# Kernel tuning notes

Measured on AMD Instinct MI355X. Metric: run time of the kernel, lower is better.

The kernel has to match this reference:

```python
import jax, jax.numpy as jnp
import numpy as np

B, T, M, DK, DV, S = 64, 256, 64, 128, 256, 128
NSK, NQ = 200, 2000


def _glorot(k, shape):
    lim = np.sqrt(6.0 / (shape[0] + shape[1])).astype(np.float32)
    return jax.random.uniform(k, shape, jnp.float32, -lim, lim)


def setup_inputs() -> dict:
    key = jax.random.key(0)
    ks = jax.random.split(key, 16)
    tn = lambda k, shape: 0.1 * jax.random.truncated_normal(k, -2.0, 2.0, shape, jnp.float32)
    return {
        "q_data": jax.random.randint(ks[0], (B, T), 0, NSK + 1),
        "qa_data": jax.random.randint(ks[1], (B, T), 0, 2 * NSK + 1),
        "s_data": jax.random.randint(ks[2], (B, T), 0, NQ + 1),
        "key_memory": tn(ks[3], (M, DK)),
        "value_memory": tn(ks[4], (M, DV)),
        "Eq": 0.05 * jax.random.normal(ks[5], (NSK + 1, DK), jnp.float32),
        "Eqa": 0.05 * jax.random.normal(ks[6], (2 * NSK + 1, DV), jnp.float32),
        "Es": 0.05 * jax.random.normal(ks[7], (NQ + 1, DK), jnp.float32),
        "We": _glorot(ks[8], (DV, DV)), "be": jnp.zeros((DV,), jnp.float32),
        "Wa": _glorot(ks[9], (DV, DV)), "ba": jnp.zeros((DV,), jnp.float32),
        "Wsa": _glorot(ks[10], (DV, M)), "bsa": jnp.zeros((M,), jnp.float32),
        "Wqd1": _glorot(ks[11], (DK, S)), "bqd1": jnp.zeros((S,), jnp.float32),
        "Wqd": _glorot(ks[12], (S, 1)), "bqd": jnp.zeros((1,), jnp.float32),
        "Wsd1": _glorot(ks[13], (DK, S)), "bsd1": jnp.zeros((S,), jnp.float32),
        "Wsd": _glorot(ks[14], (S, 1)), "bsd": jnp.zeros((1,), jnp.float32),
    }


def reference(q_data, qa_data, s_data, key_memory, value_memory, Eq, Eqa, Es,
              We, be, Wa, ba, Wsa, bsa, Wqd1, bqd1, Wqd, bqd, Wsd1, bsd1, Wsd, bsd):
    b = q_data.shape[0]
    qe = Eq[q_data]    # [B,T,DK]
    qae = Eqa[qa_data]  # [B,T,DV]
    se = Es[s_data]    # [B,T,DK]
    # time-independent precomputation (same math, hoisted out of the loop)
    corr = jax.nn.softmax(jnp.einsum("btk,mk->btm", qe, key_memory), axis=-1)  # [B,T,M]
    erase = qae @ We + be  # [B,T,DV] (activation=None in source)
    add = qae @ Wa + ba    # [B,T,DV]
    qd = jnp.tanh(qe @ Wqd1 + bqd1) @ Wqd + bqd  # [B,T,1]
    sd = jnp.tanh(se @ Wsd1 + bsd1) @ Wsd + bsd  # [B,T,1]

    def step(Mv, x):
        cw, er, ad = x  # [B,M], [B,DV], [B,DV]
        read = jnp.einsum("bm,bmd->bd", cw, Mv)        # read BEFORE write
        sa1 = read @ Wsa + bsa                          # [B,M]
        sa = jnp.sum(cw * sa1, axis=1)                  # [B]
        scale = cw[:, :, None]                          # [B,M,1]
        Mv_new = Mv * (1.0 - er[:, None, :] * scale) + ad[:, None, :] * scale
        return Mv_new, sa

    Mv0 = jnp.broadcast_to(value_memory[None], (b,) + value_memory.shape)
    xs = (corr.transpose(1, 0, 2), erase.transpose(1, 0, 2), add.transpose(1, 0, 2))
    _, sa_t = jax.lax.scan(step, Mv0, xs)  # sa_t: [T,B]
    z = 3.0 * sa_t.T - qd[..., 0] - sd[..., 0]  # [B,T]
    return jax.nn.sigmoid(z)
```

## Files before the change

kernel.cpp:

```cpp
#include <hip/hip_runtime.h>
#include <math.h>

#define B_   64
#define T_   256
#define M_   64
#define DK_  128
#define DV_  256
#define S_   128
#define NQR  201
#define NQAR 401
#define NSR  2001

static __device__ __forceinline__ int imin(int a, int b){ return a < b ? a : b; }

static __device__ __forceinline__ float fast_tanh(float x){
  float e = __expf(2.f * x);
  return 1.f - 2.f / (e + 1.f);
}

template<int CTRL, int RM>
static __device__ __forceinline__ float dppadd(float x) {
  return x + __int_as_float(
      __builtin_amdgcn_update_dpp(0, __float_as_int(x), CTRL, RM, 0xf, true));
}
static __device__ __forceinline__ float wave_sum_lane63(float x) {
  x = dppadd<0x111, 0xf>(x);
  x = dppadd<0x112, 0xf>(x);
  x = dppadd<0x114, 0xf>(x);
  x = dppadd<0x118, 0xf>(x);
  x = dppadd<0x142, 0xa>(x);
  x = dppadd<0x143, 0xc>(x);
  return x;
}
static __device__ __forceinline__ float row_sum_lane15(float x) {
  x = dppadd<0x111, 0xf>(x);
  x = dppadd<0x112, 0xf>(x);
  x = dppadd<0x114, 0xf>(x);
  x = dppadd<0x118, 0xf>(x);
  return x;
}

__device__ void corr_role(int blk, const float* __restrict__ Eq,
                          const float* __restrict__ Km,
                          const float* __restrict__ Wsa,
                          const float* __restrict__ bsa,
                          float* __restrict__ corr,
                          float* __restrict__ w2_t,
                          float* __restrict__ csb_t)
{
  __shared__ float eq[4][DK_];
  __shared__ float cwb[4][M_];
  const int w = threadIdx.x >> 6, m = threadIdx.x & 63;
  const int i  = blk * 4 + w;
  const int ic = imin(i, NQR - 1);
  eq[w][m]      = Eq[ic * DK_ + m];
  eq[w][m + 64] = Eq[ic * DK_ + 64 + m];
  float acc = 0.f;
  const float4* kr = (const float4*)(Km + m * DK_);
  #pragma unroll 8
  for (int k4 = 0; k4 < DK_ / 4; ++k4) {
    float4 kv = kr[k4];
    acc = fmaf(eq[w][k4 * 4 + 0], kv.x, acc);
    acc = fmaf(eq[w][k4 * 4 + 1], kv.y, acc);
    acc = fmaf(eq[w][k4 * 4 + 2], kv.z, acc);
    acc = fmaf(eq[w][k4 * 4 + 3], kv.w, acc);
  }
  float mx = acc;
  #pragma unroll
  for (int off = 32; off; off >>= 1) mx = fmaxf(mx, __shfl_xor(mx, off, 64));
  float e = __expf(acc - mx);
  float ssum = e;
  #pragma unroll
  for (int off = 32; off; off >>= 1) ssum += __shfl_xor(ssum, off, 64);
  const float cw = e / ssum;
  if (i < NQR) corr[i * M_ + m] = cw;
  cwb[w][m] = cw;

  float pv = wave_sum_lane63(cw * bsa[m]);
  if (m == 63 && i < NQR) csb_t[i] = pv;

  float aw[4] = {0,0,0,0};
  for (int mm4 = 0; mm4 < M_ / 4; ++mm4) {
    #pragma unroll
    for (int r = 0; r < 4; ++r) {
      float4 wv = *(const float4*)(Wsa + (r * 64 + m) * M_ + mm4 * 4);
      aw[r] = fmaf(cwb[w][mm4 * 4 + 0], wv.x, aw[r]);
      aw[r] = fmaf(cwb[w][mm4 * 4 + 1], wv.y, aw[r]);
      aw[r] = fmaf(cwb[w][mm4 * 4 + 2], wv.z, aw[r]);
      aw[r] = fmaf(cwb[w][mm4 * 4 + 3], wv.w, aw[r]);
    }
  }
  if (i < NQR) {
    #pragma unroll
    for (int r = 0; r < 4; ++r) w2_t[i * DV_ + r * 64 + m] = aw[r];
  }
}

__device__ void ea_role(int blk, const float* __restrict__ Eqa,
                        const float* __restrict__ We, const float* __restrict__ be,
                        const float* __restrict__ Wa, const float* __restrict__ ba,
                        float* __restrict__ ert, float* __restrict__ adt)
{
  __shared__ float a[8][DV_];
  const int d  = threadIdx.x;
  const int i0 = blk * 8;
  #pragma unroll
  for (int r = 0; r < 8; ++r) a[r][d] = Eqa[imin(i0 + r, NQAR - 1) * DV_ + d];
  __syncthreads();
  float er[8] = {0,0,0,0,0,0,0,0}, ad[8] = {0,0,0,0,0,0,0,0};
  for (int k = 0; k < DV_; ++k) {
    float we = We[k * DV_ + d];
    float wa = Wa[k * DV_ + d];
    #pragma unroll
    for (int r = 0; r < 8; ++r) {
      er[r] = fmaf(a[r][k], we, er[r]);
      ad[r] = fmaf(a[r][k], wa, ad[r]);
    }
  }
  const float beo = be[d], bao = ba[d];
  #pragma unroll
  for (int r = 0; r < 8; ++r) {
    int i = i0 + r;
    if (i < NQAR) { ert[i * DV_ + d] = er[r] + beo; adt[i * DV_ + d] = ad[r] + bao; }
  }
}

__device__ void mlp_role(int blk, const float* __restrict__ E,
                         const float* __restrict__ W1, const float* __restrict__ b1,
                         const float* __restrict__ W2v, const float* __restrict__ b2,
                         float* __restrict__ outt, int nrows)
{
  __shared__ float e[8 * S_];
  __shared__ float red[8][2];
  const int tid = threadIdx.x;
  const int s = tid & 127, rh = tid >> 7;
  const int i0 = blk * 8;
  #pragma unroll
  for (int j = 0; j < 4; ++j) {
    int x = tid + j * 256;
    int row = imin(i0 + (x >> 7), nrows - 1);
    e[x] = E[row * DK_ + (x & 127)];
  }
  __syncthreads();
  float acc[4] = {0,0,0,0};
  const float* eb = e + rh * 4 * 128;
  for (int k = 0; k < DK_; ++k) {
    float wv = W1[k * S_ + s];
    #pragma unroll
    for (int r = 0; r < 4; ++r) acc[r] = fmaf(eb[r * 128 + k], wv, acc[r]);
  }
  const float b1s = b1[s], w2s = W2v[s];
  float p[4];
  #pragma unroll
  for (int r = 0; r < 4; ++r) p[r] = fast_tanh(acc[r] + b1s) * w2s;
  #pragma unroll
  for (int r = 0; r < 4; ++r) p[r] = wave_sum_lane63(p[r]);
  const int lane = tid & 63;
  const int half = s >> 6;
  if (lane == 63) {
    #pragma unroll
    for (int r = 0; r < 4; ++r) red[rh * 4 + r][half] = p[r];
  }
  __syncthreads();
  if (tid < 8) {
    int i = i0 + tid;
    if (i < nrows) outt[i] = red[tid][0] + red[tid][1] + b2[0];
  }
}

#define NB_CORR 51
#define NB_EA   51
#define NB_QD   26
#define NB_SD   251
#define NB_TOT  (NB_CORR + NB_EA + NB_QD + NB_SD)

__global__ __launch_bounds__(256) void tables_kernel(
    const float* Eq, const float* Km, const float* Wsa, const float* bsa,
    float* corr_t, float* w2_t, float* csb_t,
    const float* Eqa, const float* We, const float* be,
    const float* Wa, const float* ba, float* er_t, float* ad_t,
    const float* Wqd1, const float* bqd1, const float* Wqd, const float* bqd, float* qd_t,
    const float* Es, const float* Wsd1, const float* bsd1, const float* Wsd, const float* bsd, float* sd_t)
{
  int blk = blockIdx.x;
  if (blk < NB_CORR) { corr_role(blk, Eq, Km, Wsa, bsa, corr_t, w2_t, csb_t); return; }
  blk -= NB_CORR;
  if (blk < NB_EA)   { ea_role(blk, Eqa, We, be, Wa, ba, er_t, ad_t); return; }
  blk -= NB_EA;
  if (blk < NB_QD)   { mlp_role(blk, Eq, Wqd1, bqd1, Wqd, bqd, qd_t, NQR); return; }
  blk -= NB_QD;
  mlp_role(blk, Es, Wsd1, bsd1, Wsd, bsd, sd_t, NSR);
}

struct TOps { float er, ad, w2; };

template<bool HI>
static __device__ __forceinline__ void fetch2(
    int l, const int4& qq, const int4& qaq, int m0, int d,
    const float* __restrict__ corr_t, const float* __restrict__ er_t,
    const float* __restrict__ ad_t, const float* __restrict__ w2_t,
    float4 (&c)[2][4], TOps (&o)[2])
{
  const int q0 = __builtin_amdgcn_readlane(HI ? qq.z  : qq.x,  l);
  const int q1 = __builtin_amdgcn_readlane(HI ? qq.w  : qq.y,  l);
  const int a0 = __builtin_amdgcn_readlane(HI ? qaq.z : qaq.x, l);
  const int a1 = __builtin_amdgcn_readlane(HI ? qaq.w : qaq.y, l);
  const float* cp0 = corr_t + q0 * M_ + m0;
  const float* cp1 = corr_t + q1 * M_ + m0;
  c[0][0] = *(const float4*)(cp0);
  c[0][1] = *(const float4*)(cp0 + 4);
  c[0][2] = *(const float4*)(cp0 + 8);
  c[0][3] = *(const float4*)(cp0 + 12);
  c[1][0] = *(const float4*)(cp1);
  c[1][1] = *(const float4*)(cp1 + 4);
  c[1][2] = *(const float4*)(cp1 + 8);
  c[1][3] = *(const float4*)(cp1 + 12);
  const float* e0 = er_t + a0 * DV_;
  const float* e1 = er_t + a1 * DV_;
  const float* ad0 = ad_t + a0 * DV_;
  const float* ad1 = ad_t + a1 * DV_;
  const float* w0 = w2_t + q0 * DV_;
  const float* w1 = w2_t + q1 * DV_;
  o[0].er = e0[d];  o[0].ad = ad0[d];  o[0].w2 = w0[d];
  o[1].er = e1[d];  o[1].ad = ad1[d];  o[1].w2 = w1[d];
}

static __device__ __forceinline__ float stepf(
    float (&Mv)[16], const float4 (&c)[4], const TOps& o)
{
  float r0 = c[0].x * Mv[0];
  float r1 = c[0].y * Mv[1];
  #pragma unroll
  for (int k = 0; k < 4; ++k) {
    const float cx = c[k].x, cy = c[k].y, cz = c[k].z, cw = c[k].w;
    if (k > 0) {
      r0 = fmaf(cx, Mv[4 * k + 0], r0);
      r1 = fmaf(cy, Mv[4 * k + 1], r1);
    }
    Mv[4 * k + 0] = fmaf(cx, fmaf(-o.er, Mv[4 * k + 0], o.ad), Mv[4 * k + 0]);
    Mv[4 * k + 1] = fmaf(cy, fmaf(-o.er, Mv[4 * k + 1], o.ad), Mv[4 * k + 1]);
    r0 = fmaf(cz, Mv[4 * k + 2], r0);
    r1 = fmaf(cw, Mv[4 * k + 3], r1);
    Mv[4 * k + 2] = fmaf(cz, fmaf(-o.er, Mv[4 * k + 2], o.ad), Mv[4 * k + 2]);
    Mv[4 * k + 3] = fmaf(cw, fmaf(-o.er, Mv[4 * k + 3], o.ad), Mv[4 * k + 3]);
  }
  return row_sum_lane15((r0 + r1) * o.w2);
}

__global__ __launch_bounds__(256) void scan_kernel(
    const int* __restrict__ q_data, const int* __restrict__ qa_data,
    const float* __restrict__ corr_t, const float* __restrict__ er_t,
    const float* __restrict__ ad_t, const float* __restrict__ w2_t,
    const float* __restrict__ Vm, float* __restrict__ sa_part)
{
  const int b   = blockIdx.y;
  const int dq  = blockIdx.x;
  const int tid = threadIdx.x;
  const int dl  = tid & 63;
  const int mg  = tid >> 6;
  const int m0  = __builtin_amdgcn_readfirstlane(mg * 16);
  const int d   = dq * 64 + dl;
  const int sub = dl >> 4;

  const int4 qq  = ((const int4*)(q_data  + b * T_))[dl];
  const int4 qaq = ((const int4*)(qa_data + b * T_))[dl];

  float Mv[16];
  #pragma unroll
  for (int j = 0; j < 16; ++j) Mv[j] = Vm[(m0 + j) * DV_ + d];

  float* baseP = sa_part + ((dq * 16 + mg * 4 + sub) * B_ + b) * T_;

  float4 cA[2][4], cB[2][4];
  TOps oA[2], oB[2];
  fetch2<false>(0, qq, qaq, m0, d, corr_t, er_t, ad_t, w2_t, cA, oA);
  fetch2<true >(0, qq, qaq, m0, d, corr_t, er_t, ad_t, w2_t, cB, oB);

  for (int i = 0; i < 64; ++i) {
    float4 p;
    p.x = stepf(Mv, cA[0], oA[0]);
    p.y = stepf(Mv, cA[1], oA[1]);
    fetch2<false>((i + 1) & 63, qq, qaq, m0, d, corr_t, er_t, ad_t, w2_t, cA, oA);
    p.z = stepf(Mv, cB[0], oB[0]);
    p.w = stepf(Mv, cB[1], oB[1]);
    fetch2<true >((i + 1) & 63, qq, qaq, m0, d, corr_t, er_t, ad_t, w2_t, cB, oB);
    if ((dl & 15) == 15) *(float4*)(baseP + 4 * i) = p;
  }
}

__global__ __launch_bounds__(256) void final_kernel(
    const int* __restrict__ q_data, const int* __restrict__ s_data,
    const float* __restrict__ sa_part, const float* __restrict__ csb_t,
    const float* __restrict__ qd_t, const float* __restrict__ sd_t,
    float* __restrict__ out)
{
  const int b = blockIdx.x, t = threadIdx.x;
  float s = 0.f;
  #pragma unroll
  for (int p = 0; p < 64; ++p) s += sa_part[(p * B_ + b) * T_ + t];
  const int bt = b * T_ + t;
  const int q  = q_data[bt];
  const int si = s_data[bt];
  const float sa = s + csb_t[q];
  const float z = 3.f * sa - qd_t[q] - sd_t[si];
  out[bt] = 1.f / (1.f + __expf(-z));
}

extern "C" void kernel_launch(void* const* d_in, const int* in_sizes, int n_in,
                              void* d_out, int out_size, void* d_ws, size_t ws_size,
                              hipStream_t stream)
{
  const int*   q_data = (const int*)d_in[0];
  const int*   qa_data= (const int*)d_in[1];
  const int*   s_data = (const int*)d_in[2];
  const float* Km     = (const float*)d_in[3];
  const float* Vm     = (const float*)d_in[4];
  const float* Eq     = (const float*)d_in[5];
  const float* Eqa    = (const float*)d_in[6];
  const float* Es     = (const float*)d_in[7];
  const float* We     = (const float*)d_in[8];
  const float* be     = (const float*)d_in[9];
  const float* Wa     = (const float*)d_in[10];
  const float* ba     = (const float*)d_in[11];
  const float* Wsa    = (const float*)d_in[12];
  const float* bsa    = (const float*)d_in[13];
  const float* Wqd1   = (const float*)d_in[14];
  const float* bqd1   = (const float*)d_in[15];
  const float* Wqd    = (const float*)d_in[16];
  const float* bqd    = (const float*)d_in[17];
  const float* Wsd1   = (const float*)d_in[18];
  const float* bsd1   = (const float*)d_in[19];
  const float* Wsd    = (const float*)d_in[20];
  const float* bsd    = (const float*)d_in[21];
  float* out = (float*)d_out;

  float* wsf    = (float*)d_ws;
  float* corr_t = wsf;
  float* w2_t   = corr_t + NQR * M_;
  float* csb_t  = w2_t + NQR * DV_;
  float* er_t   = csb_t + 204;
  float* ad_t   = er_t + NQAR * DV_;
  float* qd_t   = ad_t + NQAR * DV_;
  float* sd_t   = qd_t + 204;
  float* sa_p   = sd_t + 2004;

  tables_kernel<<<NB_TOT, 256, 0, stream>>>(
      Eq, Km, Wsa, bsa, corr_t, w2_t, csb_t,
      Eqa, We, be, Wa, ba, er_t, ad_t,
      Wqd1, bqd1, Wqd, bqd, qd_t,
      Es, Wsd1, bsd1, Wsd, bsd, sd_t);
  scan_kernel<<<dim3(4, B_), 256, 0, stream>>>(q_data, qa_data, corr_t, er_t, ad_t, w2_t, Vm, sa_p);
  final_kernel<<<B_, 256, 0, stream>>>(q_data, s_data, sa_p, csb_t, qd_t, sd_t, out);
}
```

Measured before the change: 178.5 us.

## Interleave erase/add tables, pack index pairs, deepen scan prefetch pipeline

```diff
diff --git a/kernel.cpp b/kernel.cpp
--- a/kernel.cpp
+++ b/kernel.cpp
@@ -99,7 +99,7 @@
 __device__ void ea_role(int blk, const float* __restrict__ Eqa,
                         const float* __restrict__ We, const float* __restrict__ be,
                         const float* __restrict__ Wa, const float* __restrict__ ba,
-                        float* __restrict__ ert, float* __restrict__ adt)
+                        float* __restrict__ eat)
 {
   __shared__ float a[8][DV_];
   const int d  = threadIdx.x;
@@ -121,7 +121,10 @@
   #pragma unroll
   for (int r = 0; r < 8; ++r) {
     int i = i0 + r;
-    if (i < NQAR) { ert[i * DV_ + d] = er[r] + beo; adt[i * DV_ + d] = ad[r] + bao; }
+    if (i < NQAR) {
+      float2 v; v.x = er[r] + beo; v.y = ad[r] + bao;
+      *(float2*)(eat + (size_t)(i * DV_ + d) * 2) = v;
+    }
   }
 }
 
@@ -168,66 +171,96 @@
   }
 }
 
+__device__ void pk_role(int blk, const int* __restrict__ q,
+                        const int* __restrict__ qa, int* __restrict__ pkt)
+{
+  const int i = (blk * 256 + threadIdx.x) * 4;
+  int4 qv = *(const int4*)(q + i);
+  int4 av = *(const int4*)(qa + i);
+  int4 p;
+  p.x = (av.x << 16) | qv.x;
+  p.y = (av.y << 16) | qv.y;
+  p.z = (av.z << 16) | qv.z;
+  p.w = (av.w << 16) | qv.w;
+  *(int4*)(pkt + i) = p;
+}
+
 #define NB_CORR 51
 #define NB_EA   51
 #define NB_QD   26
 #define NB_SD   251
-#define NB_TOT  (NB_CORR + NB_EA + NB_QD + NB_SD)
+#define NB_PK   16
+#define NB_TOT  (NB_CORR + NB_EA + NB_QD + NB_SD + NB_PK)
 
 __global__ __launch_bounds__(256) void tables_kernel(
+    const int* q_data, const int* qa_data, int* pkt,
     const float* Eq, const float* Km, const float* Wsa, const float* bsa,
     float* corr_t, float* w2_t, float* csb_t,
     const float* Eqa, const float* We, const float* be,
-    const float* Wa, const float* ba, float* er_t, float* ad_t,
+    const float* Wa, const float* ba, float* eat,
     const float* Wqd1, const float* bqd1, const float* Wqd, const float* bqd, float* qd_t,
     const float* Es, const float* Wsd1, const float* bsd1, const float* Wsd, const float* bsd, float* sd_t)
 {
   int blk = blockIdx.x;
   if (blk < NB_CORR) { corr_role(blk, Eq, Km, Wsa, bsa, corr_t, w2_t, csb_t); return; }
   blk -= NB_CORR;
-  if (blk < NB_EA)   { ea_role(blk, Eqa, We, be, Wa, ba, er_t, ad_t); return; }
+  if (blk < NB_EA)   { ea_role(blk, Eqa, We, be, Wa, ba, eat); return; }
   blk -= NB_EA;
   if (blk < NB_QD)   { mlp_role(blk, Eq, Wqd1, bqd1, Wqd, bqd, qd_t, NQR); return; }
   blk -= NB_QD;
-  mlp_role(blk, Es, Wsd1, bsd1, Wsd, bsd, sd_t, NSR);
-}
-
-struct TOps { float er, ad, w2; };
-
-template<bool HI>
-static __device__ __forceinline__ void fetch2(
-    int l, const int4& qq, const int4& qaq, int m0, int d,
-    const float* __restrict__ corr_t, const float* __restrict__ er_t,
-    const float* __restrict__ ad_t, const float* __restrict__ w2_t,
-    float4 (&c)[2][4], TOps (&o)[2])
-{
-  const int q0 = __builtin_amdgcn_readlane(HI ? qq.z  : qq.x,  l);
-  const int q1 = __builtin_amdgcn_readlane(HI ? qq.w  : qq.y,  l);
-  const int a0 = __builtin_amdgcn_readlane(HI ? qaq.z : qaq.x, l);
-  const int a1 = __builtin_amdgcn_readlane(HI ? qaq.w : qaq.y, l);
-  const float* cp0 = corr_t + q0 * M_ + m0;
-  const float* cp1 = corr_t + q1 * M_ + m0;
-  c[0][0] = *(const float4*)(cp0);
-  c[0][1] = *(const float4*)(cp0 + 4);
-  c[0][2] = *(const float4*)(cp0 + 8);
-  c[0][3] = *(const float4*)(cp0 + 12);
-  c[1][0] = *(const float4*)(cp1);
-  c[1][1] = *(const float4*)(cp1 + 4);
-  c[1][2] = *(const float4*)(cp1 + 8);
-  c[1][3] = *(const float4*)(cp1 + 12);
-  const float* e0 = er_t + a0 * DV_;
-  const float* e1 = er_t + a1 * DV_;
-  const float* ad0 = ad_t + a0 * DV_;
-  const float* ad1 = ad_t + a1 * DV_;
-  const float* w0 = w2_t + q0 * DV_;
-  const float* w1 = w2_t + q1 * DV_;
-  o[0].er = e0[d];  o[0].ad = ad0[d];  o[0].w2 = w0[d];
-  o[1].er = e1[d];  o[1].ad = ad1[d];  o[1].w2 = w1[d];
+  if (blk < NB_SD)   { mlp_role(blk, Es, Wsd1, bsd1, Wsd, bsd, sd_t, NSR); return; }
+  blk -= NB_SD;
+  pk_role(blk, q_data, qa_data, pkt);
+}
+
+struct VOps { float2 ea0, ea1; float w20, w21; };
+
+static __device__ __forceinline__ int4 getpk(const int4& pk, int g) {
+  int4 r;
+  r.x = __builtin_amdgcn_readlane(pk.x, g);
+  r.y = __builtin_amdgcn_readlane(pk.y, g);
+  r.z = __builtin_amdgcn_readlane(pk.z, g);
+  r.w = __builtin_amdgcn_readlane(pk.w, g);
+  return r;
+}
+#define PQ(v)  ((v) & 0xffff)
+#define PA(v)  ((int)(((unsigned)(v)) >> 16))
+
+static __device__ __forceinline__ void fetch_c(
+    const int4& P, int m0, const float* __restrict__ corr_t,
+    float4 (&cA)[2][4], float4 (&cB)[2][4])
+{
+  const float4* p0 = (const float4*)(corr_t + PQ(P.x) * M_ + m0);
+  const float4* p1 = (const float4*)(corr_t + PQ(P.y) * M_ + m0);
+  const float4* p2 = (const float4*)(corr_t + PQ(P.z) * M_ + m0);
+  const float4* p3 = (const float4*)(corr_t + PQ(P.w) * M_ + m0);
+  #pragma unroll
+  for (int k = 0; k < 4; ++k) {
+    cA[0][k] = p0[k];
+    cA[1][k] = p1[k];
+    cB[0][k] = p2[k];
+    cB[1][k] = p3[k];
+  }
+}
+
+static __device__ __forceinline__ void fetch_v(
+    const int4& P, int d, const float* __restrict__ eat,
+    const float* __restrict__ w2_t, VOps& A, VOps& B)
+{
+  A.ea0 = *(const float2*)(eat + (size_t)(PA(P.x) * DV_ + d) * 2);
+  A.ea1 = *(const float2*)(eat + (size_t)(PA(P.y) * DV_ + d) * 2);
+  B.ea0 = *(const float2*)(eat + (size_t)(PA(P.z) * DV_ + d) * 2);
+  B.ea1 = *(const float2*)(eat + (size_t)(PA(P.w) * DV_ + d) * 2);
+  A.w20 = w2_t[PQ(P.x) * DV_ + d];
+  A.w21 = w2_t[PQ(P.y) * DV_ + d];
+  B.w20 = w2_t[PQ(P.z) * DV_ + d];
+  B.w21 = w2_t[PQ(P.w) * DV_ + d];
 }
 
 static __device__ __forceinline__ float stepf(
-    float (&Mv)[16], const float4 (&c)[4], const TOps& o)
-{
+    float (&Mv)[16], const float4 (&c)[4], float2 ea, float w2)
+{
+  const float er = ea.x, ad = ea.y;
   float r0 = c[0].x * Mv[0];
   float r1 = c[0].y * Mv[1];
   #pragma unroll
@@ -237,20 +270,20 @@
       r0 = fmaf(cx, Mv[4 * k + 0], r0);
       r1 = fmaf(cy, Mv[4 * k + 1], r1);
     }
-    Mv[4 * k + 0] = fmaf(cx, fmaf(-o.er, Mv[4 * k + 0], o.ad), Mv[4 * k + 0]);
-    Mv[4 * k + 1] = fmaf(cy, fmaf(-o.er, Mv[4 * k + 1], o.ad), Mv[4 * k + 1]);
+    Mv[4 * k + 0] = fmaf(cx, fmaf(-er, Mv[4 * k + 0], ad), Mv[4 * k + 0]);
+    Mv[4 * k + 1] = fmaf(cy, fmaf(-er, Mv[4 * k + 1], ad), Mv[4 * k + 1]);
     r0 = fmaf(cz, Mv[4 * k + 2], r0);
     r1 = fmaf(cw, Mv[4 * k + 3], r1);
-    Mv[4 * k + 2] = fmaf(cz, fmaf(-o.er, Mv[4 * k + 2], o.ad), Mv[4 * k + 2]);
-    Mv[4 * k + 3] = fmaf(cw, fmaf(-o.er, Mv[4 * k + 3], o.ad), Mv[4 * k + 3]);
-  }
-  return row_sum_lane15((r0 + r1) * o.w2);
+    Mv[4 * k + 2] = fmaf(cz, fmaf(-er, Mv[4 * k + 2], ad), Mv[4 * k + 2]);
+    Mv[4 * k + 3] = fmaf(cw, fmaf(-er, Mv[4 * k + 3], ad), Mv[4 * k + 3]);
+  }
+  return row_sum_lane15((r0 + r1) * w2);
 }
 
 __global__ __launch_bounds__(256) void scan_kernel(
-    const int* __restrict__ q_data, const int* __restrict__ qa_data,
-    const float* __restrict__ corr_t, const float* __restrict__ er_t,
-    const float* __restrict__ ad_t, const float* __restrict__ w2_t,
+    const int* __restrict__ pkt,
+    const float* __restrict__ corr_t, const float* __restrict__ eat,
+    const float* __restrict__ w2_t,
     const float* __restrict__ Vm, float* __restrict__ sa_part)
 {
   const int b   = blockIdx.y;
@@ -262,8 +295,7 @@
   const int d   = dq * 64 + dl;
   const int sub = dl >> 4;
 
-  const int4 qq  = ((const int4*)(q_data  + b * T_))[dl];
-  const int4 qaq = ((const int4*)(qa_data + b * T_))[dl];
+  const int4 pk = ((const int4*)(pkt + b * T_))[dl];
 
   float Mv[16];
   #pragma unroll
@@ -271,20 +303,37 @@
 
   float* baseP = sa_part + ((dq * 16 + mg * 4 + sub) * B_ + b) * T_;
 
+  int4 I0 = getpk(pk, 0);
+  int4 I1 = getpk(pk, 1);
   float4 cA[2][4], cB[2][4];
-  TOps oA[2], oB[2];
-  fetch2<false>(0, qq, qaq, m0, d, corr_t, er_t, ad_t, w2_t, cA, oA);
-  fetch2<true >(0, qq, qaq, m0, d, corr_t, er_t, ad_t, w2_t, cB, oB);
-
-  for (int i = 0; i < 64; ++i) {
+  VOps VEa, VEb, VOa, VOb;
+  fetch_c(I0, m0, corr_t, cA, cB);
+  fetch_v(I0, d, eat, w2_t, VEa, VEb);
+  fetch_v(I1, d, eat, w2_t, VOa, VOb);
+  int4 Icur = I1;
+  int4 Inxt = getpk(pk, 2);
+
+  for (int i = 0; i < 64; i += 2) {
     float4 p;
-    p.x = stepf(Mv, cA[0], oA[0]);
-    p.y = stepf(Mv, cA[1], oA[1]);
-    fetch2<false>((i + 1) & 63, qq, qaq, m0, d, corr_t, er_t, ad_t, w2_t, cA, oA);
-    p.z = stepf(Mv, cB[0], oB[0]);
-    p.w = stepf(Mv, cB[1], oB[1]);
-    fetch2<true >((i + 1) & 63, qq, qaq, m0, d, corr_t, er_t, ad_t, w2_t, cB, oB);
+    p.x = stepf(Mv, cA[0], VEa.ea0, VEa.w20);
+    p.y = stepf(Mv, cA[1], VEa.ea1, VEa.w21);
+    p.z = stepf(Mv, cB[0], VEb.ea0, VEb.w20);
+    p.w = stepf(Mv, cB[1], VEb.ea1, VEb.w21);
+    fetch_c(Icur, m0, corr_t, cA, cB);
+    fetch_v(Inxt, d, eat, w2_t, VEa, VEb);
+    Icur = Inxt;
+    Inxt = getpk(pk, (i + 3) & 63);
     if ((dl & 15) == 15) *(float4*)(baseP + 4 * i) = p;
+
+    p.x = stepf(Mv, cA[0], VOa.ea0, VOa.w20);
+    p.y = stepf(Mv, cA[1], VOa.ea1, VOa.w21);
+    p.z = stepf(Mv, cB[0], VOb.ea0, VOb.w20);
+    p.w = stepf(Mv, cB[1], VOb.ea1, VOb.w21);
+    fetch_c(Icur, m0, corr_t, cA, cB);
+    fetch_v(Inxt, d, eat, w2_t, VOa, VOb);
+    Icur = Inxt;
+    Inxt = getpk(pk, (i + 4) & 63);
+    if ((dl & 15) == 15) *(float4*)(baseP + 4 * i + 4) = p;
   }
 }
 
@@ -338,17 +387,18 @@
   float* corr_t = wsf;
   float* w2_t   = corr_t + NQR * M_;
   float* csb_t  = w2_t + NQR * DV_;
-  float* er_t   = csb_t + 204;
-  float* ad_t   = er_t + NQAR * DV_;
-  float* qd_t   = ad_t + NQAR * DV_;
+  float* eat    = csb_t + 204;
+  float* qd_t   = eat + NQAR * DV_ * 2;
   float* sd_t   = qd_t + 204;
-  float* sa_p   = sd_t + 2004;
+  int*   pkt    = (int*)(sd_t + 2004);
+  float* sa_p   = sd_t + 2004 + 16384;
 
   tables_kernel<<<NB_TOT, 256, 0, stream>>>(
+      q_data, qa_data, pkt,
       Eq, Km, Wsa, bsa, corr_t, w2_t, csb_t,
-      Eqa, We, be, Wa, ba, er_t, ad_t,
+      Eqa, We, be, Wa, ba, eat,
       Wqd1, bqd1, Wqd, bqd, qd_t,
       Es, Wsd1, bsd1, Wsd, bsd, sd_t);
-  scan_kernel<<<dim3(4, B_), 256, 0, stream>>>(q_data, qa_data, corr_t, er_t, ad_t, w2_t, Vm, sa_p);
+  scan_kernel<<<dim3(4, B_), 256, 0, stream>>>(pkt, corr_t, eat, w2_t, Vm, sa_p);
   final_kernel<<<B_, 256, 0, stream>>>(q_data, s_data, sa_p, csb_t, qd_t, sd_t, out);
 }
```

Result: faster. 165.5 us (-7.3%).
